# Performance work log

Hardware: AMD Instinct MI355X
Metric: run time of the kernel (lower is better)

## Reference

```python
import jax, jax.numpy as jnp
import numpy as np

SEARCH_RANGE = 4  # matches args.search_range


def _displacements(r):
    # Exact channel ordering of the original double loop:
    # I=0 -> (0,0); then for i=1..r: (-i,0),(+i,0),(0,-i),(0,+i),
    # then for j=1..r: (-i,-j),(+i,+j),(-i,+j),(+i,-j).
    ds = [(0, 0)]
    for i in range(1, r + 1):
        ds += [(-i, 0), (i, 0), (0, -i), (0, i)]
        for j in range(1, r + 1):
            ds += [(-i, -j), (i, j), (-i, j), (i, -j)]
    return ds


def setup_inputs() -> dict:
    key = jax.random.key(0)
    k1, k2 = jax.random.split(key)
    B, C, H, W = 4, 128, 96, 160
    src = jax.random.normal(k1, (B, C, H, W), dtype=jnp.float32)
    tgt = jax.random.normal(k2, (B, C, H, W), dtype=jnp.float32)
    return {"src": src, "tgt": tgt}


def reference(src, tgt):
    r = SEARCH_RANGE
    B, C, H, W = src.shape
    D = (2 * r + 1) ** 2  # 81 displacement channels
    # Zero-pad tgt spatially so out-of-range shifted regions contribute 0,
    # matching the torch version's zero-initialized output slices.
    tgt_pad = jnp.pad(tgt, ((0, 0), (0, 0), (r, r), (r, r)))
    chans = []
    for dy, dx in _displacements(r):
        # shifted[b,c,y,x] = tgt[b,c,y+dy,x+dx] (0 outside)
        t = jax.lax.dynamic_slice(tgt_pad, (0, 0, r + dy, r + dx), (B, C, H, W))
        chans.append(jnp.einsum('bchw,bchw->bhw', src, t))
    out = jnp.stack(chans, axis=1)  # [B, D, H, W]
    return out / D
```

## Files before the change

kernel.cpp:

```cpp
#include <hip/hip_runtime.h>
#include <hip/hip_bf16.h>

#define BATCH 4
#define CHAN 128
#define HGT 96
#define WID 160
#define HW (HGT * WID)
#define THREADS 512
#define TENSOR_ELEMS (BATCH * CHAN * HGT * WID)
#define WS_NEED ((size_t)TENSOR_ELEMS * 2)

typedef __attribute__((ext_vector_type(8))) short short8;
typedef __attribute__((ext_vector_type(4))) float float4v;

__device__ __forceinline__ int chan_of(int dy, int dx) {
    if (dy == 0 && dx == 0) return 0;
    if (dx == 0) { int i = dy < 0 ? -dy : dy; return 1 + (i - 1) * 20 + (dy < 0 ? 0 : 1); }
    if (dy == 0) { int i = dx < 0 ? -dx : dx; return 1 + (i - 1) * 20 + (dx < 0 ? 2 : 3); }
    int i = dy < 0 ? -dy : dy;
    int j = dx < 0 ? -dx : dx;
    int s = (dy < 0) ? (dx < 0 ? 0 : 2) : (dx < 0 ? 3 : 1);
    return 1 + (i - 1) * 20 + 4 + (j - 1) * 4 + s;
}

__device__ __forceinline__ unsigned pk2(float a, float b) {
    __hip_bfloat162 h = __float22bfloat162_rn(make_float2(a, b));
    unsigned u;
    __builtin_memcpy(&u, &h, 4);
    return u;
}

union sl_u { uint4 v; short8 s; };

__global__ __launch_bounds__(256)
void nhwc_bf16_tgt(const float* __restrict__ tgt, ushort* __restrict__ ws) {
    __shared__ unsigned s_t[64][65];
    int r = blockIdx.x;
    const int xb = r % 3; r /= 3;
    const int y  = r % HGT; r /= HGT;
    const int b  = r;
    const int x0 = xb * 64;
    const int npx = (x0 + 64 <= WID) ? 64 : (WID - x0);

    const int t  = threadIdx.x;
    const int x1 = t & 63, cp0 = t >> 6;
    if (x1 < npx) {
        const int base = (b * CHAN * HGT + y) * WID + x0 + x1;
        #pragma unroll
        for (int i = 0; i < 16; ++i) {
            const int cp = cp0 + i * 4;
            s_t[cp][x1] = pk2(tgt[base + (2 * cp) * HW],
                              tgt[base + (2 * cp + 1) * HW]);
        }
    }
    __syncthreads();
    const int x2 = t >> 2, g = t & 3;
    if (x2 < npx) {
        ushort* op = ws + ((size_t)(b * HGT + y) * WID + x0 + x2) * CHAN + g * 32;
        #pragma unroll
        for (int k = 0; k < 4; ++k) {
            uint4 v;
            v.x = s_t[g * 16 + k * 4 + 0][x2];
            v.y = s_t[g * 16 + k * 4 + 1][x2];
            v.z = s_t[g * 16 + k * 4 + 2][x2];
            v.w = s_t[g * 16 + k * 4 + 3][x2];
            *(uint4*)(op + k * 8) = v;
        }
    }
}

__global__ __launch_bounds__(THREADS, 4)
void cost_volume_mfma(const float* __restrict__ src,
                      const ushort* __restrict__ tgtT,
                      float* __restrict__ out) {
    __shared__ __align__(16) uint4 s_b[4736];
    __shared__ int s_tab[81];

    const int tid  = threadIdx.x;
    const int wv   = tid >> 6;
    const int wvy  = wv & 3;
    const int wvd  = wv >> 2;
    const int lane = tid & 63;
    const int q    = lane >> 4;
    const int ln   = lane & 15;

    const int w    = blockIdx.x;
    const int slab = w & 7;
    const int b    = slab >> 1;
    const int yh   = slab & 1;
    const int t    = w >> 3;
    const int x0   = (t % 10) * 16;
    const int y0   = yh * 48 + (t / 10) * 4;

    if (tid < 81) s_tab[tid] = chan_of(tid / 9 - 4, tid % 9 - 4) * HW;

    const int y = y0 + wvy;
    const int sbase = (b * CHAN * HGT + y) * WID + x0 + ln + q * 8 * HW;
    float apay[32];
    #pragma unroll
    for (int ks = 0; ks < 4; ++ks)
        #pragma unroll
        for (int j = 0; j < 8; ++j)
            apay[ks * 8 + j] = src[sbase + (ks * 32 + j) * HW];

    const ushort* tbase = tgtT + (size_t)b * HGT * WID * CHAN;
    #pragma unroll
    for (int k = 0; k < 9; ++k) {
        const int u   = k * THREADS + tid;
        const int j   = u & 15;
        const int v16 = u >> 4;
        const int row = v16 / 24;
        const int x   = v16 - row * 24;
        const int gr  = y0 - 4 + row;
        const int gx  = x0 - 4 + x;
        const int oct = j ^ (x & 15);
        unsigned* lp = (unsigned*)&s_b[k * THREADS + (tid & ~63)];
        if (((unsigned)gr < (unsigned)HGT) && ((unsigned)gx < (unsigned)WID)) {
            const unsigned* gp =
                (const unsigned*)(tbase + ((gr * WID + gx) * CHAN + oct * 8));
            __builtin_amdgcn_global_load_lds(gp, lp, 16, 0, 0);
        } else {
            s_b[u] = make_uint4(0u, 0u, 0u, 0u);
        }
    }

    __builtin_amdgcn_sched_barrier(0);
    __syncthreads();

    short8 afr[4];
    #pragma unroll
    for (int ks = 0; ks < 4; ++ks) {
        sl_u f;
        f.v.x = pk2(apay[ks * 8 + 0], apay[ks * 8 + 1]);
        f.v.y = pk2(apay[ks * 8 + 2], apay[ks * 8 + 3]);
        f.v.z = pk2(apay[ks * 8 + 4], apay[ks * 8 + 5]);
        f.v.w = pk2(apay[ks * 8 + 6], apay[ks * 8 + 7]);
        afr[ks] = f.s;
    }

    float4v aa0[5], aa1[5];
    #define COMPUTE_DY(DD, DYI)                                               \
        {                                                                     \
            const int rr = wvy + (DYI);                                       \
            float4v a0 = (float4v){0.f, 0.f, 0.f, 0.f};                       \
            float4v a1 = (float4v){0.f, 0.f, 0.f, 0.f};                       \
            _Pragma("unroll")                                                 \
            for (int ks = 0; ks < 4; ++ks) {                                  \
                sl_u b0;                                    \
                b0.v = s_b[(rr * 24 + ln) * 16 + ((q + ks * 4) ^ ln)];        \
                a0 = __builtin_amdgcn_mfma_f32_16x16x32_bf16(afr[ks], b0.s, a0, 0, 0, 0); \
            }                                                                 \
            _Pragma("unroll")                                                 \
            for (int ks = 0; ks < 4; ++ks) {                                  \
                sl_u b1;                                 \
                b1.v = s_b[(rr * 24 + 16 + ln) * 16 + ((q + ks * 4) ^ ln)];   \
                a1 = __builtin_amdgcn_mfma_f32_16x16x32_bf16(afr[ks], b1.s, a1, 0, 0, 0); \
            }                                                                 \
            aa0[DD] = a0; aa1[DD] = a1;                                       \
        }
    if (wvd == 0) {
        #pragma unroll
        for (int dd = 0; dd < 4; ++dd) COMPUTE_DY(dd, dd)
    } else {
        #pragma unroll
        for (int dd = 0; dd < 5; ++dd) COMPUTE_DY(dd, dd + 4)
    }

    __syncthreads();

    float* s_o = (float*)s_b;
    const float inv = 1.0f / 81.0f;
    #define EPI_DY(DD, DYI)                                                   \
        _Pragma("unroll")                                                     \
        for (int reg = 0; reg < 4; ++reg) {                                   \
            const int m = q * 4 + reg;                                        \
            const int t0x = ln - m;                        \
            if ((unsigned)t0x <= 8u)                                          \
                s_o[((DYI) * 9 + t0x) * 68 + wvy * 16 + m] = aa0[DD][reg] * inv; \
            const int t1x = ln + 16 - m;                   \
            if ((unsigned)t1x <= 8u)                                          \
                s_o[((DYI) * 9 + t1x) * 68 + wvy * 16 + m] = aa1[DD][reg] * inv; \
        }
    if (wvd == 0) {
        #pragma unroll
        for (int dd = 0; dd < 4; ++dd) EPI_DY(dd, dd)
    } else {
        #pragma unroll
        for (int dd = 0; dd < 5; ++dd) EPI_DY(dd, dd + 4)
    }
    __syncthreads();

    const size_t ob = (size_t)b * 81 * HW + (size_t)y0 * WID + x0;
    #pragma unroll
    for (int it = 0; it < 3; ++it) {
        const int v = it * THREADS + tid;
        if (v < 1296) {
            const int xq  = v & 3;
            const int row = v >> 2;
            const int cix = row >> 2;
            const int yy  = row & 3;
            float4v val = *(const float4v*)&s_o[cix * 68 + yy * 16 + xq * 4];
            *(float4v*)&out[ob + s_tab[cix] + yy * WID + xq * 4] = val;
        }
    }
}

#define FST_DECODE(TAG, U)                                                    \
    const int u##TAG   = (U);                                                 \
    const int xq##TAG  = u##TAG % 6;                                          \
    const int r6##TAG  = u##TAG / 6;                                          \
    const int oct##TAG = r6##TAG & 15;                                        \
    const int row##TAG = r6##TAG >> 4;                                        \
    const int gr##TAG  = y0 - 4 + row##TAG;                                   \
    const int gx##TAG  = x0 - 4 + xq##TAG * 4;                                \
    const bool ok##TAG = ((unsigned)gr##TAG < (unsigned)HGT) &&               \
                         ((unsigned)gx##TAG < (unsigned)WID);                 \
    const int ga##TAG  = tb + (oct##TAG * 8 * HGT + gr##TAG) * WID + gx##TAG;

#define FST_ISSUE(TAG, COND)                                                  \
    _Pragma("unroll")                                                         \
    for (int j = 0; j < 8; ++j)                                               \
        p##TAG[j] = (COND) ? *(const float4v*)(tgt + ga##TAG + j * HW)        \
                           : (float4v){0.f, 0.f, 0.f, 0.f};

#define FST_WRITE(TAG)                                                        \
    _Pragma("unroll")                                                         \
    for (int i = 0; i < 4; ++i) {                                             \
        const int xl = xq##TAG * 4 + i;                                       \
        uint4 val;                                                            \
        val.x = pk2(p##TAG[0][i], p##TAG[1][i]);                              \
        val.y = pk2(p##TAG[2][i], p##TAG[3][i]);                              \
        val.z = pk2(p##TAG[4][i], p##TAG[5][i]);                              \
        val.w = pk2(p##TAG[6][i], p##TAG[7][i]);                              \
        s_b[(row##TAG * 24 + xl) * 16 + (oct##TAG ^ (xl & 15))] = val;        \
    }

__global__ __launch_bounds__(THREADS, 4)
void cost_volume_fused(const float* __restrict__ src,
                       const float* __restrict__ tgt,
                       float* __restrict__ out) {
    __shared__ __align__(16) uint4 s_b[4736];
    __shared__ int s_tab[81];

    const int tid  = threadIdx.x;
    const int wv   = tid >> 6;
    const int wvy  = wv & 3;
    const int wvd  = wv >> 2;
    const int lane = tid & 63;
    const int q    = lane >> 4;
    const int ln   = lane & 15;

    const int w    = blockIdx.x;
    const int slab = w & 7;
    const int b    = slab >> 1;
    const int yh   = slab & 1;
    const int t    = w >> 3;
    const int x0   = (t % 10) * 16;
    const int y0   = yh * 48 + (t / 10) * 4;

    if (tid < 81) s_tab[tid] = chan_of(tid / 9 - 4, tid % 9 - 4) * HW;

    const int tb = b * CHAN * HGT * WID;

    FST_DECODE(0, tid)
    FST_DECODE(1, tid + 512)
    FST_DECODE(2, tid + 1024)
    const bool has2 = tid < 128;

    float4v p0[8], p1[8], p2[8];
    FST_ISSUE(0, ok0)

    const int y = y0 + wvy;
    const int sbase = (b * CHAN * HGT + y) * WID + x0 + ln + q * 8 * HW;
    float apay[32];
    #pragma unroll
    for (int ks = 0; ks < 4; ++ks)
        #pragma unroll
        for (int j = 0; j < 8; ++j)
            apay[ks * 8 + j] = src[sbase + (ks * 32 + j) * HW];

    FST_ISSUE(1, ok1)
    FST_WRITE(0)
    FST_ISSUE(2, has2 && ok2)
    short8 afr[4];
    #pragma unroll
    for (int ks = 0; ks < 4; ++ks) {
        sl_u f;
        f.v.x = pk2(apay[ks * 8 + 0], apay[ks * 8 + 1]);
        f.v.y = pk2(apay[ks * 8 + 2], apay[ks * 8 + 3]);
        f.v.z = pk2(apay[ks * 8 + 4], apay[ks * 8 + 5]);
        f.v.w = pk2(apay[ks * 8 + 6], apay[ks * 8 + 7]);
        afr[ks] = f.s;
    }
    FST_WRITE(1)
    if (has2) { FST_WRITE(2) }

    __syncthreads();

    float4v aa0[5], aa1[5];
    if (wvd == 0) {
        #pragma unroll
        for (int dd = 0; dd < 4; ++dd) COMPUTE_DY(dd, dd)
    } else {
        #pragma unroll
        for (int dd = 0; dd < 5; ++dd) COMPUTE_DY(dd, dd + 4)
    }

    __syncthreads();

    float* s_o = (float*)s_b;
    const float inv = 1.0f / 81.0f;
    if (wvd == 0) {
        #pragma unroll
        for (int dd = 0; dd < 4; ++dd) EPI_DY(dd, dd)
    } else {
        #pragma unroll
        for (int dd = 0; dd < 5; ++dd) EPI_DY(dd, dd + 4)
    }
    __syncthreads();

    const size_t ob = (size_t)b * 81 * HW + (size_t)y0 * WID + x0;
    #pragma unroll
    for (int it = 0; it < 3; ++it) {
        const int v = it * THREADS + tid;
        if (v < 1296) {
            const int xq  = v & 3;
            const int row = v >> 2;
            const int cix = row >> 2;
            const int yy  = row & 3;
            float4v val = *(const float4v*)&s_o[cix * 68 + yy * 16 + xq * 4];
            *(float4v*)&out[ob + s_tab[cix] + yy * WID + xq * 4] = val;
        }
    }
}

extern "C" void kernel_launch(void* const* d_in, const int* in_sizes, int n_in,
                              void* d_out, int out_size, void* d_ws, size_t ws_size,
                              hipStream_t stream) {
    const float* src = (const float*)d_in[0];
    const float* tgt = (const float*)d_in[1];
    float* out = (float*)d_out;
    if (d_ws && ws_size >= WS_NEED) {
        ushort* ws = (ushort*)d_ws;
        nhwc_bf16_tgt<<<dim3(1152, 1, 1), dim3(256, 1, 1), 0, stream>>>(tgt, ws);
        cost_volume_mfma<<<dim3(960, 1, 1), dim3(THREADS, 1, 1), 0, stream>>>(src, ws, out);
    } else {
        cost_volume_fused<<<dim3(960, 1, 1), dim3(THREADS, 1, 1), 0, stream>>>(src, tgt, out);
    }
}
```

Measured before the change: 117.5 us.

## Load target B-fragments directly from global memory instead of staging in LDS

Drops the LDS staging of the 12x24 halo tile of transposed bf16 target and its barrier. Each wave now reads its MFMA B operands straight from global/L2 per displacement row, with bounds checks replaced by zero fragments. This frees LDS (only the output staging buffer remains), which may allow higher occupancy, and removes the async LDS load plus sync. The cost is redundant global reads, since neighbouring waves and blocks re-fetch overlapping target rows.

```diff
diff --git a/kernel.cpp b/kernel.cpp
--- a/kernel.cpp
+++ b/kernel.cpp
@@ -70,10 +70,10 @@
 }
 
 __global__ __launch_bounds__(THREADS, 4)
-void cost_volume_mfma(const float* __restrict__ src,
-                      const ushort* __restrict__ tgtT,
-                      float* __restrict__ out) {
-    __shared__ __align__(16) uint4 s_b[4736];
+void cost_volume_direct(const float* __restrict__ src,
+                        const ushort* __restrict__ tgtT,
+                        float* __restrict__ out) {
+    __shared__ float s_o[81 * 68];
     __shared__ int s_tab[81];
 
     const int tid  = threadIdx.x;
@@ -102,31 +102,6 @@
         #pragma unroll
         for (int j = 0; j < 8; ++j)
             apay[ks * 8 + j] = src[sbase + (ks * 32 + j) * HW];
-
-    const ushort* tbase = tgtT + (size_t)b * HGT * WID * CHAN;
-    #pragma unroll
-    for (int k = 0; k < 9; ++k) {
-        const int u   = k * THREADS + tid;
-        const int j   = u & 15;
-        const int v16 = u >> 4;
-        const int row = v16 / 24;
-        const int x   = v16 - row * 24;
-        const int gr  = y0 - 4 + row;
-        const int gx  = x0 - 4 + x;
-        const int oct = j ^ (x & 15);
-        unsigned* lp = (unsigned*)&s_b[k * THREADS + (tid & ~63)];
-        if (((unsigned)gr < (unsigned)HGT) && ((unsigned)gx < (unsigned)WID)) {
-            const unsigned* gp =
-                (const unsigned*)(tbase + ((gr * WID + gx) * CHAN + oct * 8));
-            __builtin_amdgcn_global_load_lds(gp, lp, 16, 0, 0);
-        } else {
-            s_b[u] = make_uint4(0u, 0u, 0u, 0u);
-        }
-    }
-
-    __builtin_amdgcn_sched_barrier(0);
-    __syncthreads();
-
     short8 afr[4];
     #pragma unroll
     for (int ks = 0; ks < 4; ++ks) {
@@ -138,55 +113,59 @@
         afr[ks] = f.s;
     }
 
+    const ushort* tb8 = tgtT + (size_t)b * HGT * WID * CHAN;
+    const int gx0 = x0 - 4 + ln;
+    const int gx1 = x0 + 12 + ln;
+    const bool cok0 = (unsigned)gx0 < (unsigned)WID;
+    const bool cok1 = (unsigned)gx1 < (unsigned)WID;
+    const short8 zf = (short8){0, 0, 0, 0, 0, 0, 0, 0};
+
     float4v aa0[5], aa1[5];
-    #define COMPUTE_DY(DD, DYI)                                               \
-        {                                                                     \
-            const int rr = wvy + (DYI);                                       \
-            float4v a0 = (float4v){0.f, 0.f, 0.f, 0.f};                       \
-            float4v a1 = (float4v){0.f, 0.f, 0.f, 0.f};                       \
-            _Pragma("unroll")                                                 \
-            for (int ks = 0; ks < 4; ++ks) {                                  \
-                sl_u b0;                                    \
-                b0.v = s_b[(rr * 24 + ln) * 16 + ((q + ks * 4) ^ ln)];        \
-                a0 = __builtin_amdgcn_mfma_f32_16x16x32_bf16(afr[ks], b0.s, a0, 0, 0, 0); \
-            }                                                                 \
-            _Pragma("unroll")                                                 \
-            for (int ks = 0; ks < 4; ++ks) {                                  \
-                sl_u b1;                                 \
-                b1.v = s_b[(rr * 24 + 16 + ln) * 16 + ((q + ks * 4) ^ ln)];   \
-                a1 = __builtin_amdgcn_mfma_f32_16x16x32_bf16(afr[ks], b1.s, a1, 0, 0, 0); \
-            }                                                                 \
-            aa0[DD] = a0; aa1[DD] = a1;                                       \
-        }
-    if (wvd == 0) {
-        #pragma unroll
-        for (int dd = 0; dd < 4; ++dd) COMPUTE_DY(dd, dd)
-    } else {
-        #pragma unroll
-        for (int dd = 0; dd < 5; ++dd) COMPUTE_DY(dd, dd + 4)
-    }
-
-    __syncthreads();
-
-    float* s_o = (float*)s_b;
+    const int ndd = wvd ? 5 : 4;
+    #pragma unroll
+    for (int dd = 0; dd < 5; ++dd) {
+        if (dd >= ndd) break;
+        const int dyi = wvd ? dd + 4 : dd;
+        const int gr  = y0 - 4 + wvy + dyi;
+        float4v a0 = (float4v){0.f, 0.f, 0.f, 0.f};
+        float4v a1 = (float4v){0.f, 0.f, 0.f, 0.f};
+        if ((unsigned)gr < (unsigned)HGT) {
+            const ushort* rp = tb8 + (size_t)gr * WID * CHAN;
+            const ushort* p0 = rp + gx0 * CHAN + q * 8;
+            const ushort* p1 = rp + gx1 * CHAN + q * 8;
+            short8 bf0[4], bf1[4];
+            #pragma unroll
+            for (int ks = 0; ks < 4; ++ks)
+                bf0[ks] = cok0 ? *(const short8*)(p0 + ks * 32) : zf;
+            #pragma unroll
+            for (int ks = 0; ks < 4; ++ks)
+                bf1[ks] = cok1 ? *(const short8*)(p1 + ks * 32) : zf;
+            #pragma unroll
+            for (int ks = 0; ks < 4; ++ks)
+                a0 = __builtin_amdgcn_mfma_f32_16x16x32_bf16(afr[ks], bf0[ks], a0, 0, 0, 0);
+            #pragma unroll
+            for (int ks = 0; ks < 4; ++ks)
+                a1 = __builtin_amdgcn_mfma_f32_16x16x32_bf16(afr[ks], bf1[ks], a1, 0, 0, 0);
+        }
+        aa0[dd] = a0;
+        aa1[dd] = a1;
+    }
+
     const float inv = 1.0f / 81.0f;
-    #define EPI_DY(DD, DYI)                                                   \
-        _Pragma("unroll")                                                     \
-        for (int reg = 0; reg < 4; ++reg) {                                   \
-            const int m = q * 4 + reg;                                        \
-            const int t0x = ln - m;                        \
-            if ((unsigned)t0x <= 8u)                                          \
-                s_o[((DYI) * 9 + t0x) * 68 + wvy * 16 + m] = aa0[DD][reg] * inv; \
-            const int t1x = ln + 16 - m;                   \
-            if ((unsigned)t1x <= 8u)                                          \
-                s_o[((DYI) * 9 + t1x) * 68 + wvy * 16 + m] = aa1[DD][reg] * inv; \
-        }
-    if (wvd == 0) {
-        #pragma unroll
-        for (int dd = 0; dd < 4; ++dd) EPI_DY(dd, dd)
-    } else {
-        #pragma unroll
-        for (int dd = 0; dd < 5; ++dd) EPI_DY(dd, dd + 4)
+    #pragma unroll
+    for (int dd = 0; dd < 5; ++dd) {
+        if (dd >= ndd) break;
+        const int dyi = wvd ? dd + 4 : dd;
+        #pragma unroll
+        for (int reg = 0; reg < 4; ++reg) {
+            const int m = q * 4 + reg;
+            const int t0x = ln - m;
+            if ((unsigned)t0x <= 8u)
+                s_o[(dyi * 9 + t0x) * 68 + wvy * 16 + m] = aa0[dd][reg] * inv;
+            const int t1x = ln + 16 - m;
+            if ((unsigned)t1x <= 8u)
+                s_o[(dyi * 9 + t1x) * 68 + wvy * 16 + m] = aa1[dd][reg] * inv;
+        }
     }
     __syncthreads();
 
@@ -298,6 +277,25 @@
     __syncthreads();
 
     float4v aa0[5], aa1[5];
+    #define COMPUTE_DY(DD, DYI)                                               \
+        {                                                                     \
+            const int rr = wvy + (DYI);                                       \
+            float4v a0 = (float4v){0.f, 0.f, 0.f, 0.f};                       \
+            float4v a1 = (float4v){0.f, 0.f, 0.f, 0.f};                       \
+            _Pragma("unroll")                                                 \
+            for (int ks = 0; ks < 4; ++ks) {                                  \
+                sl_u b0;                                                      \
+                b0.v = s_b[(rr * 24 + ln) * 16 + ((q + ks * 4) ^ ln)];        \
+                a0 = __builtin_amdgcn_mfma_f32_16x16x32_bf16(afr[ks], b0.s, a0, 0, 0, 0); \
+            }                                                                 \
+            _Pragma("unroll")                                                 \
+            for (int ks = 0; ks < 4; ++ks) {                                  \
+                sl_u b1;                                                      \
+                b1.v = s_b[(rr * 24 + 16 + ln) * 16 + ((q + ks * 4) ^ ln)];   \
+                a1 = __builtin_amdgcn_mfma_f32_16x16x32_bf16(afr[ks], b1.s, a1, 0, 0, 0); \
+            }                                                                 \
+            aa0[DD] = a0; aa1[DD] = a1;                                       \
+        }
     if (wvd == 0) {
         #pragma unroll
         for (int dd = 0; dd < 4; ++dd) COMPUTE_DY(dd, dd)
@@ -310,6 +308,17 @@
 
     float* s_o = (float*)s_b;
     const float inv = 1.0f / 81.0f;
+    #define EPI_DY(DD, DYI)                                                   \
+        _Pragma("unroll")                                                     \
+        for (int reg = 0; reg < 4; ++reg) {                                   \
+            const int m = q * 4 + reg;                                        \
+            const int t0x = ln - m;                                           \
+            if ((unsigned)t0x <= 8u)                                          \
+                s_o[((DYI) * 9 + t0x) * 68 + wvy * 16 + m] = aa0[DD][reg] * inv; \
+            const int t1x = ln + 16 - m;                                      \
+            if ((unsigned)t1x <= 8u)                                          \
+                s_o[((DYI) * 9 + t1x) * 68 + wvy * 16 + m] = aa1[DD][reg] * inv; \
+        }
     if (wvd == 0) {
         #pragma unroll
         for (int dd = 0; dd < 4; ++dd) EPI_DY(dd, dd)
@@ -343,7 +352,7 @@
     if (d_ws && ws_size >= WS_NEED) {
         ushort* ws = (ushort*)d_ws;
         nhwc_bf16_tgt<<<dim3(1152, 1, 1), dim3(256, 1, 1), 0, stream>>>(tgt, ws);
-        cost_volume_mfma<<<dim3(960, 1, 1), dim3(THREADS, 1, 1), 0, stream>>>(src, ws, out);
+        cost_volume_direct<<<dim3(960, 1, 1), dim3(THREADS, 1, 1), 0, stream>>>(src, ws, out);
     } else {
         cost_volume_fused<<<dim3(960, 1, 1), dim3(THREADS, 1, 1), 0, stream>>>(src, tgt, out);
     }
```

After: 138.1 us. 1.18x slower.

## Read bf16 target operands directly from global memory instead of staging in LDS

Applied to the files above, without the earlier changes.

The workspace path's cost-volume kernel no longer stages a target halo tile into shared memory. Each wave now loads its MFMA B fragments straight from the NHWC bf16 workspace (relying on cache for reuse across waves), with column masking, and skips rows outside the image. This removes the bulk LDS fill and one barrier, at the cost of more global or L2 traffic and exposed load latency per MFMA group. The fallback fused kernel also gets a modified LDS swizzle for the right half-tile, scheduling barriers, and lower launch bounds, but that path only runs without a workspace.

```diff
diff --git a/kernel.cpp b/kernel.cpp
--- a/kernel.cpp
+++ b/kernel.cpp
@@ -69,11 +69,49 @@
     }
 }
 
+#define DIR_DY(DD, DYI)                                                       \
+    {                                                                         \
+        const int gr = y0 - 4 + wvy + (DYI);            \
+        float4v a0 = (float4v){0.f, 0.f, 0.f, 0.f};                           \
+        float4v a1 = (float4v){0.f, 0.f, 0.f, 0.f};                           \
+        if ((unsigned)gr < (unsigned)HGT) {                                   \
+            const ushort* rp  = tb8 + (size_t)gr * WID * CHAN;                \
+            const ushort* pp0 = rp + gx0 * CHAN + q * 8;                      \
+            const ushort* pp1 = rp + gx1 * CHAN + q * 8;                      \
+            short8 bf0[4], bf1[4];                                            \
+            _Pragma("unroll")                                                 \
+            for (int ks = 0; ks < 4; ++ks)                                    \
+                bf0[ks] = cok0 ? *(const short8*)(pp0 + ks * 32) : zf;        \
+            _Pragma("unroll")                                                 \
+            for (int ks = 0; ks < 4; ++ks)                                    \
+                bf1[ks] = cok1 ? *(const short8*)(pp1 + ks * 32) : zf;        \
+            _Pragma("unroll")                                                 \
+            for (int ks = 0; ks < 4; ++ks)                                    \
+                a0 = __builtin_amdgcn_mfma_f32_16x16x32_bf16(afr[ks], bf0[ks], a0, 0, 0, 0); \
+            _Pragma("unroll")                                                 \
+            for (int ks = 0; ks < 4; ++ks)                                    \
+                a1 = __builtin_amdgcn_mfma_f32_16x16x32_bf16(afr[ks], bf1[ks], a1, 0, 0, 0); \
+        }                                                                     \
+        aa0[DD] = a0; aa1[DD] = a1;                                           \
+    }
+
+#define EPID_DY(DD, DYI)                                                      \
+    _Pragma("unroll")                                                         \
+    for (int reg = 0; reg < 4; ++reg) {                                       \
+        const int m = q * 4 + reg;                                            \
+        const int t0x = ln - m;                            \
+        if ((unsigned)t0x <= 8u)                                              \
+            s_o[((DYI) * 9 + t0x) * 68 + wvy * 16 + m] = aa0[DD][reg] * inv;  \
+        const int t1x = ln + 16 - m;                       \
+        if ((unsigned)t1x <= 8u)                                              \
+            s_o[((DYI) * 9 + t1x) * 68 + wvy * 16 + m] = aa1[DD][reg] * inv;  \
+    }
+
 __global__ __launch_bounds__(THREADS, 4)
-void cost_volume_mfma(const float* __restrict__ src,
-                      const ushort* __restrict__ tgtT,
-                      float* __restrict__ out) {
-    __shared__ __align__(16) uint4 s_b[4736];
+void cost_volume_direct(const float* __restrict__ src,
+                        const ushort* __restrict__ tgtT,
+                        float* __restrict__ out) {
+    __shared__ float s_o[81 * 68];
     __shared__ int s_tab[81];
 
     const int tid  = threadIdx.x;
@@ -102,31 +140,6 @@
         #pragma unroll
         for (int j = 0; j < 8; ++j)
             apay[ks * 8 + j] = src[sbase + (ks * 32 + j) * HW];
-
-    const ushort* tbase = tgtT + (size_t)b * HGT * WID * CHAN;
-    #pragma unroll
-    for (int k = 0; k < 9; ++k) {
-        const int u   = k * THREADS + tid;
-        const int j   = u & 15;
-        const int v16 = u >> 4;
-        const int row = v16 / 24;
-        const int x   = v16 - row * 24;
-        const int gr  = y0 - 4 + row;
-        const int gx  = x0 - 4 + x;
-        const int oct = j ^ (x & 15);
-        unsigned* lp = (unsigned*)&s_b[k * THREADS + (tid & ~63)];
-        if (((unsigned)gr < (unsigned)HGT) && ((unsigned)gx < (unsigned)WID)) {
-            const unsigned* gp =
-                (const unsigned*)(tbase + ((gr * WID + gx) * CHAN + oct * 8));
-            __builtin_amdgcn_global_load_lds(gp, lp, 16, 0, 0);
-        } else {
-            s_b[u] = make_uint4(0u, 0u, 0u, 0u);
-        }
-    }
-
-    __builtin_amdgcn_sched_barrier(0);
-    __syncthreads();
-
     short8 afr[4];
     #pragma unroll
     for (int ks = 0; ks < 4; ++ks) {
@@ -138,55 +151,27 @@
         afr[ks] = f.s;
     }
 
+    const ushort* tb8 = tgtT + (size_t)b * HGT * WID * CHAN;
+    const int gx0 = x0 - 4 + ln;
+    const int gx1 = x0 + 12 + ln;
+    const bool cok0 = (unsigned)gx0 < (unsigned)WID;
+    const bool cok1 = (unsigned)gx1 < (unsigned)WID;
+    const short8 zf = (short8){0, 0, 0, 0, 0, 0, 0, 0};
+
     float4v aa0[5], aa1[5];
-    #define COMPUTE_DY(DD, DYI)                                               \
-        {                                                                     \
-            const int rr = wvy + (DYI);                                       \
-            float4v a0 = (float4v){0.f, 0.f, 0.f, 0.f};                       \
-            float4v a1 = (float4v){0.f, 0.f, 0.f, 0.f};                       \
-            _Pragma("unroll")                                                 \
-            for (int ks = 0; ks < 4; ++ks) {                                  \
-                sl_u b0;                                    \
-                b0.v = s_b[(rr * 24 + ln) * 16 + ((q + ks * 4) ^ ln)];        \
-                a0 = __builtin_amdgcn_mfma_f32_16x16x32_bf16(afr[ks], b0.s, a0, 0, 0, 0); \
-            }                                                                 \
-            _Pragma("unroll")                                                 \
-            for (int ks = 0; ks < 4; ++ks) {                                  \
-                sl_u b1;                                 \
-                b1.v = s_b[(rr * 24 + 16 + ln) * 16 + ((q + ks * 4) ^ ln)];   \
-                a1 = __builtin_amdgcn_mfma_f32_16x16x32_bf16(afr[ks], b1.s, a1, 0, 0, 0); \
-            }                                                                 \
-            aa0[DD] = a0; aa1[DD] = a1;                                       \
-        }
     if (wvd == 0) {
-        #pragma unroll
-        for (int dd = 0; dd < 4; ++dd) COMPUTE_DY(dd, dd)
-    } else {
-        #pragma unroll
-        for (int dd = 0; dd < 5; ++dd) COMPUTE_DY(dd, dd + 4)
-    }
-
-    __syncthreads();
-
-    float* s_o = (float*)s_b;
+        DIR_DY(0, 0) DIR_DY(1, 1) DIR_DY(2, 2) DIR_DY(3, 3)
+        aa0[4] = (float4v){0.f, 0.f, 0.f, 0.f};
+        aa1[4] = (float4v){0.f, 0.f, 0.f, 0.f};
+    } else {
+        DIR_DY(0, 4) DIR_DY(1, 5) DIR_DY(2, 6) DIR_DY(3, 7) DIR_DY(4, 8)
+    }
+
     const float inv = 1.0f / 81.0f;
-    #define EPI_DY(DD, DYI)                                                   \
-        _Pragma("unroll")                                                     \
-        for (int reg = 0; reg < 4; ++reg) {                                   \
-            const int m = q * 4 + reg;                                        \
-            const int t0x = ln - m;                        \
-            if ((unsigned)t0x <= 8u)                                          \
-                s_o[((DYI) * 9 + t0x) * 68 + wvy * 16 + m] = aa0[DD][reg] * inv; \
-            const int t1x = ln + 16 - m;                   \
-            if ((unsigned)t1x <= 8u)                                          \
-                s_o[((DYI) * 9 + t1x) * 68 + wvy * 16 + m] = aa1[DD][reg] * inv; \
-        }
     if (wvd == 0) {
-        #pragma unroll
-        for (int dd = 0; dd < 4; ++dd) EPI_DY(dd, dd)
-    } else {
-        #pragma unroll
-        for (int dd = 0; dd < 5; ++dd) EPI_DY(dd, dd + 4)
+        EPID_DY(0, 0) EPID_DY(1, 1) EPID_DY(2, 2) EPID_DY(3, 3)
+    } else {
+        EPID_DY(0, 4) EPID_DY(1, 5) EPID_DY(2, 6) EPID_DY(3, 7) EPID_DY(4, 8)
     }
     __syncthreads();
 
@@ -232,10 +217,43 @@
         val.y = pk2(p##TAG[2][i], p##TAG[3][i]);                              \
         val.z = pk2(p##TAG[4][i], p##TAG[5][i]);                              \
         val.w = pk2(p##TAG[6][i], p##TAG[7][i]);                              \
-        s_b[(row##TAG * 24 + xl) * 16 + (oct##TAG ^ (xl & 15))] = val;        \
-    }
-
-__global__ __launch_bounds__(THREADS, 4)
+        s_b[(row##TAG * 24 + xl) * 16 +                                       \
+            (oct##TAG ^ (xl & 15) ^ ((xl >> 4) << 3))] = val;                 \
+    }
+
+#define COMPUTE_DY(DD, DYI)                                                   \
+    {                                                                         \
+        const int rr = wvy + (DYI);                                           \
+        float4v a0 = (float4v){0.f, 0.f, 0.f, 0.f};                           \
+        float4v a1 = (float4v){0.f, 0.f, 0.f, 0.f};                           \
+        _Pragma("unroll")                                                     \
+        for (int ks = 0; ks < 4; ++ks) {                                      \
+            sl_u b0;                                                          \
+            b0.v = s_b[(rr * 24 + ln) * 16 + ((q + ks * 4) ^ ln)];            \
+            a0 = __builtin_amdgcn_mfma_f32_16x16x32_bf16(afr[ks], b0.s, a0, 0, 0, 0); \
+        }                                                                     \
+        _Pragma("unroll")                                                     \
+        for (int ks = 0; ks < 4; ++ks) {                                      \
+            sl_u b1;                                                          \
+            b1.v = s_b[(rr * 24 + 16 + ln) * 16 + (((q + ks * 4) ^ ln) ^ 8)]; \
+            a1 = __builtin_amdgcn_mfma_f32_16x16x32_bf16(afr[ks], b1.s, a1, 0, 0, 0); \
+        }                                                                     \
+        aa0[DD] = a0; aa1[DD] = a1;                                           \
+    }
+
+#define EPI_DY(DD, DYI)                                                       \
+    _Pragma("unroll")                                                         \
+    for (int reg = 0; reg < 4; ++reg) {                                       \
+        const int m = q * 4 + reg;                                            \
+        const int t0x = ln - m;                                               \
+        if ((unsigned)t0x <= 8u)                                              \
+            s_o[((DYI) * 9 + t0x) * 68 + wvy * 16 + m] = aa0[DD][reg] * inv;  \
+        const int t1x = ln + 16 - m;                                          \
+        if ((unsigned)t1x <= 8u)                                              \
+            s_o[((DYI) * 9 + t1x) * 68 + wvy * 16 + m] = aa1[DD][reg] * inv;  \
+    }
+
+__global__ __launch_bounds__(THREADS, 2)
 void cost_volume_fused(const float* __restrict__ src,
                        const float* __restrict__ tgt,
                        float* __restrict__ out) {
@@ -280,8 +298,10 @@
             apay[ks * 8 + j] = src[sbase + (ks * 32 + j) * HW];
 
     FST_ISSUE(1, ok1)
+    __builtin_amdgcn_sched_barrier(0);
     FST_WRITE(0)
     FST_ISSUE(2, has2 && ok2)
+    __builtin_amdgcn_sched_barrier(0);
     short8 afr[4];
     #pragma unroll
     for (int ks = 0; ks < 4; ++ks) {
@@ -293,17 +313,16 @@
         afr[ks] = f.s;
     }
     FST_WRITE(1)
+    __builtin_amdgcn_sched_barrier(0);
     if (has2) { FST_WRITE(2) }
-
+    __builtin_amdgcn_sched_barrier(0);
     __syncthreads();
 
     float4v aa0[5], aa1[5];
     if (wvd == 0) {
-        #pragma unroll
-        for (int dd = 0; dd < 4; ++dd) COMPUTE_DY(dd, dd)
-    } else {
-        #pragma unroll
-        for (int dd = 0; dd < 5; ++dd) COMPUTE_DY(dd, dd + 4)
+        COMPUTE_DY(0, 0) COMPUTE_DY(1, 1) COMPUTE_DY(2, 2) COMPUTE_DY(3, 3)
+    } else {
+        COMPUTE_DY(0, 4) COMPUTE_DY(1, 5) COMPUTE_DY(2, 6) COMPUTE_DY(3, 7) COMPUTE_DY(4, 8)
     }
 
     __syncthreads();
@@ -311,11 +330,9 @@
     float* s_o = (float*)s_b;
     const float inv = 1.0f / 81.0f;
     if (wvd == 0) {
-        #pragma unroll
-        for (int dd = 0; dd < 4; ++dd) EPI_DY(dd, dd)
-    } else {
-        #pragma unroll
-        for (int dd = 0; dd < 5; ++dd) EPI_DY(dd, dd + 4)
+        EPI_DY(0, 0) EPI_DY(1, 1) EPI_DY(2, 2) EPI_DY(3, 3)
+    } else {
+        EPI_DY(0, 4) EPI_DY(1, 5) EPI_DY(2, 6) EPI_DY(3, 7) EPI_DY(4, 8)
     }
     __syncthreads();
 
@@ -343,7 +360,7 @@
     if (d_ws && ws_size >= WS_NEED) {
         ushort* ws = (ushort*)d_ws;
         nhwc_bf16_tgt<<<dim3(1152, 1, 1), dim3(256, 1, 1), 0, stream>>>(tgt, ws);
-        cost_volume_mfma<<<dim3(960, 1, 1), dim3(THREADS, 1, 1), 0, stream>>>(src, ws, out);
+        cost_volume_direct<<<dim3(960, 1, 1), dim3(THREADS, 1, 1), 0, stream>>>(src, ws, out);
     } else {
         cost_volume_fused<<<dim3(960, 1, 1), dim3(THREADS, 1, 1), 0, stream>>>(src, tgt, out);
     }
```

Result: slower. 140.8 us (+19.8%).
